# Kernel tuning notes

Hardware: AMD Instinct MI355X
Metric: run time of the kernel (lower is better)

## Reference

```python
import jax, jax.numpy as jnp
import numpy as np

DIM = 512
NUM_HEADS = 8
HEAD_DIM = DIM // NUM_HEADS
SCALE = HEAD_DIM ** -0.5


def setup_inputs() -> dict:
    key = jax.random.key(0)
    k_x, k_qkv, k_proj, k_pb = jax.random.split(key, 4)
    x = jax.random.normal(k_x, (2, 4096, DIM), dtype=jnp.float32)
    # nn.Linear weights: stored as [out, in]; qkv_bias=False so no qkv bias.
    w_qkv = jax.random.normal(k_qkv, (3 * DIM, DIM), dtype=jnp.float32) * (DIM ** -0.5)
    w_proj = jax.random.normal(k_proj, (DIM, DIM), dtype=jnp.float32) * (DIM ** -0.5)
    b_proj = jax.random.normal(k_pb, (DIM,), dtype=jnp.float32) * 0.01
    return {"x": x, "w_qkv": w_qkv, "w_proj": w_proj, "b_proj": b_proj}


def reference(x, w_qkv, w_proj, b_proj):
    B, N, D = x.shape
    H, Hd = NUM_HEADS, HEAD_DIM
    # qkv: [B, N, 3D] -> [3, B, H, N, Hd]
    qkv = (x @ w_qkv.T).reshape(B, N, 3, H, Hd).transpose(2, 0, 3, 1, 4)
    q, k, v = qkv[0], qkv[1], qkv[2]
    # Naive full attention matrix in fp32 (matches original non-fused path).
    attn = jnp.einsum('bhqd,bhkd->bhqk', q, k) * SCALE
    attn = jax.nn.softmax(attn, axis=-1)
    out = jnp.einsum('bhqk,bhkd->bhqd', attn, v)
    out = out.transpose(0, 2, 1, 3).reshape(B, N, D)
    return out @ w_proj.T + b_proj
```

## Files before the change

kernel.cpp:

```cpp
#include <hip/hip_runtime.h>
#include <stdint.h>

#define SEQ   4096
#define DIMM  512
#define HDIM  64
#define NH    8
#define ROWS  8192
#define QKVN  1536

typedef __attribute__((ext_vector_type(8))) __bf16 bf16x8;
typedef __attribute__((ext_vector_type(4))) float  f32x4;
typedef __attribute__((ext_vector_type(2))) uint32_t u32x2;

__device__ __forceinline__ uint16_t f2bfu(float f) {
  uint32_t u = __builtin_bit_cast(uint32_t, f);
  return (uint16_t)((u + 0x7FFFu + ((u >> 16) & 1u)) >> 16);
}

__device__ __forceinline__ f32x4 mfma16(bf16x8 a, bf16x8 b, f32x4 c) {
  return __builtin_amdgcn_mfma_f32_16x16x32_bf16(a, b, c, 0, 0, 0);
}

__device__ __forceinline__ void gld16(const void* g, void* l) {
  __builtin_amdgcn_global_load_lds(
      (const __attribute__((address_space(1))) uint32_t*)g,
      (__attribute__((address_space(3))) uint32_t*)l, 16, 0, 0);
}

#define X4  (ROWS * DIMM / 4)
#define Q4  (QKVN * DIMM / 4)
#define P4  (DIMM * DIMM / 4)

__global__ __launch_bounds__(256) void cvt_kernel(
    const float* __restrict__ x, const float* __restrict__ wq,
    const float* __restrict__ wp, uint16_t* __restrict__ xb,
    uint16_t* __restrict__ wqb, uint16_t* __restrict__ wpb) {
  int idx = blockIdx.x * 256 + threadIdx.x;
  const float* src; uint16_t* dst; int i4;
  if (idx < X4)            { src = x;  dst = xb;  i4 = idx; }
  else if (idx < X4 + Q4)  { src = wq; dst = wqb; i4 = idx - X4; }
  else                     { src = wp; dst = wpb; i4 = idx - X4 - Q4; }
  float4 v = ((const float4*)src)[i4];
  ushort4 o;
  o.x = f2bfu(v.x); o.y = f2bfu(v.y); o.z = f2bfu(v.z); o.w = f2bfu(v.w);
  ((ushort4*)dst)[i4] = o;
}

__device__ __forceinline__ void gemm_core(
    const uint16_t* __restrict__ A, const uint16_t* __restrict__ B,
    uint16_t* As, uint16_t* Bs, f32x4 acc[4][4]) {
  const int tid = threadIdx.x;
  const int lane = tid & 63, wave = tid >> 6;
  const int quad = lane >> 4, l16 = lane & 15;
  const int wr = (wave & 1) * 64, wc = (wave >> 1) * 64;
  const int bm = blockIdx.x, bn = blockIdx.y;
  const int sw = (l16 >> 1) & 3;

  for (int kt = 0; kt < DIMM / 32; ++kt) {
#pragma unroll
    for (int it = 0; it < 2; ++it) {
      int L = it * 256 + tid;
      int r = L >> 2, c = L & 3;
      int gc = c ^ ((r >> 1) & 3);
      int ldsoff = (it * 256 + (tid & ~63)) * 16;
      gld16((const char*)A + ((size_t)(bm * 128 + r) * DIMM + kt * 32) * 2 + gc * 16,
            (char*)As + ldsoff);
      gld16((const char*)B + ((size_t)(bn * 128 + r) * DIMM + kt * 32) * 2 + gc * 16,
            (char*)Bs + ldsoff);
    }
    __syncthreads();
    bf16x8 af[4], bfr[4];
#pragma unroll
    for (int i = 0; i < 4; ++i)
      af[i] = *(const bf16x8*)(As + (wr + i * 16 + l16) * 32 + ((quad ^ sw) * 8));
#pragma unroll
    for (int j = 0; j < 4; ++j)
      bfr[j] = *(const bf16x8*)(Bs + (wc + j * 16 + l16) * 32 + ((quad ^ sw) * 8));
#pragma unroll
    for (int i = 0; i < 4; ++i)
#pragma unroll
      for (int j = 0; j < 4; ++j)
        acc[i][j] = mfma16(af[i], bfr[j], acc[i][j]);
    __syncthreads();
  }
}

__global__ __launch_bounds__(256, 2) void qkv_gemm(
    const uint16_t* __restrict__ xb, const uint16_t* __restrict__ wqb,
    uint16_t* __restrict__ qd, uint16_t* __restrict__ kd,
    uint16_t* __restrict__ vt) {
  __shared__ __align__(16) uint16_t As[128 * 32];
  __shared__ __align__(16) uint16_t Bs[128 * 32];
  f32x4 acc[4][4];
#pragma unroll
  for (int i = 0; i < 4; ++i)
#pragma unroll
    for (int j = 0; j < 4; ++j) acc[i][j] = f32x4{0.f, 0.f, 0.f, 0.f};

  gemm_core(xb, wqb, As, Bs, acc);

  const int lane = threadIdx.x & 63, wave = threadIdx.x >> 6;
  const int quad = lane >> 4, l16 = lane & 15;
  const int wr = (wave & 1) * 64, wc = (wave >> 1) * 64;
#pragma unroll
  for (int i = 0; i < 4; ++i) {
    int m0 = blockIdx.x * 128 + wr + i * 16 + quad * 4;
    int b = m0 >> 12, n0 = m0 & 4095;
#pragma unroll
    for (int j = 0; j < 4; ++j) {
      int jc = blockIdx.y * 128 + wc + j * 16 + l16;
      int region = jc >> 9;
      int h = (jc >> 6) & 7, hd = jc & 63;
      int bh = (b << 3) | h;
      if (region == 0) {
#pragma unroll
        for (int r = 0; r < 4; ++r)
          qd[((size_t)bh * SEQ + n0 + r) * HDIM + hd] = f2bfu(acc[i][j][r] * 0.125f);
      } else if (region == 1) {
#pragma unroll
        for (int r = 0; r < 4; ++r)
          kd[((size_t)bh * SEQ + n0 + r) * HDIM + hd] = f2bfu(acc[i][j][r]);
      } else {
        ushort4 pk;
        pk.x = f2bfu(acc[i][j][0]); pk.y = f2bfu(acc[i][j][1]);
        pk.z = f2bfu(acc[i][j][2]); pk.w = f2bfu(acc[i][j][3]);
        *(ushort4*)(vt + ((size_t)bh * HDIM + hd) * SEQ + n0) = pk;
      }
    }
  }
}

__global__ __launch_bounds__(256, 3) void attn_kernel(
    const uint16_t* __restrict__ qd, const uint16_t* __restrict__ kd,
    const uint16_t* __restrict__ vt, uint16_t* __restrict__ ao) {
  __shared__ __align__(16) uint16_t Ks[128 * 64];
  __shared__ __align__(16) uint16_t Vs[64 * 128];
  __shared__ __align__(16) uint16_t Ps[4][32 * 64];

  const int tid = threadIdx.x, lane = tid & 63, wave = tid >> 6;
  const int quad = lane >> 4, l16 = lane & 15;
  const int qt = blockIdx.x, bh = blockIdx.y;
  const size_t base_qk = (size_t)bh * SEQ * HDIM;
  const size_t base_v  = (size_t)bh * HDIM * SEQ;
  const int sw7 = l16 & 7;
  uint16_t* Pw = &Ps[wave][0];

  bf16x8 qf[2][2];
#pragma unroll
  for (int it2 = 0; it2 < 2; ++it2)
#pragma unroll
    for (int kh = 0; kh < 2; ++kh)
      qf[it2][kh] = *(const bf16x8*)(qd + base_qk +
          (size_t)(qt * 128 + wave * 32 + it2 * 16 + l16) * HDIM + kh * 32 + quad * 8);

  f32x4 O[2][4];
  float lsum[2] = {0.f, 0.f};
#pragma unroll
  for (int a = 0; a < 2; ++a)
#pragma unroll
    for (int d = 0; d < 4; ++d) O[a][d] = f32x4{0.f, 0.f, 0.f, 0.f};

  for (int kt = 0; kt < SEQ / 128; ++kt) {
#pragma unroll
    for (int it = 0; it < 4; ++it) {
      int L = it * 256 + tid;
      int ldsoff = (it * 256 + (tid & ~63)) * 16;
      int rk = L >> 3, ck = L & 7;
      int gck = ck ^ (rk & 7);
      gld16((const char*)kd + (base_qk + (size_t)(kt * 128 + rk) * HDIM) * 2 + gck * 16,
            (char*)Ks + ldsoff);
      int rv = L >> 4, cv = L & 15;
      int gcv = cv ^ (rv & 15);
      gld16((const char*)vt + (base_v + (size_t)rv * SEQ + (size_t)kt * 128) * 2 + gcv * 16,
            (char*)Vs + ldsoff);
    }
    __syncthreads();

#pragma unroll
    for (int half = 0; half < 2; ++half) {
      f32x4 P[4][2];
#pragma unroll
      for (int jh = 0; jh < 4; ++jh) {
        int jf = half * 4 + jh;
        const uint16_t* krow = Ks + (jf * 16 + l16) * 64;
        bf16x8 kf0 = *(const bf16x8*)(krow + ((quad ^ sw7) * 8));
        bf16x8 kf1 = *(const bf16x8*)(krow + (((4 + quad) ^ sw7) * 8));
#pragma unroll
        for (int it2 = 0; it2 < 2; ++it2) {
          f32x4 s = f32x4{0.f, 0.f, 0.f, 0.f};
          s = mfma16(kf0, qf[it2][0], s);
          s = mfma16(kf1, qf[it2][1], s);
          P[jh][it2] = s;
        }
      }

#pragma unroll
      for (int jh = 0; jh < 4; ++jh)
#pragma unroll
        for (int it2 = 0; it2 < 2; ++it2) {
          float p0 = __expf(P[jh][it2][0]);
          float p1 = __expf(P[jh][it2][1]);
          float p2 = __expf(P[jh][it2][2]);
          float p3 = __expf(P[jh][it2][3]);
          lsum[it2] += (p0 + p1) + (p2 + p3);
          uint32_t a0 = __builtin_bit_cast(uint32_t, p0) + 0x8000u;
          uint32_t a1 = __builtin_bit_cast(uint32_t, p1) + 0x8000u;
          uint32_t a2 = __builtin_bit_cast(uint32_t, p2) + 0x8000u;
          uint32_t a3 = __builtin_bit_cast(uint32_t, p3) + 0x8000u;
          u32x2 pk;
          pk.x = (a0 >> 16) | (a1 & 0xFFFF0000u);
          pk.y = (a2 >> 16) | (a3 & 0xFFFF0000u);
          int c16 = (jh * 2 + (quad >> 1)) ^ sw7;
          *(u32x2*)((char*)Pw + (it2 * 16 + l16) * 128 + c16 * 16 + (quad & 1) * 8) = pk;
        }

#pragma unroll
      for (int kp = 0; kp < 2; ++kp) {
        bf16x8 pb[2];
#pragma unroll
        for (int it2 = 0; it2 < 2; ++it2)
          pb[it2] = *(const bf16x8*)((const char*)Pw + (it2 * 16 + l16) * 128 +
                                     (((kp * 4 + quad) ^ sw7) * 16));
        bf16x8 va[4];
#pragma unroll
        for (int dl = 0; dl < 4; ++dl)
          va[dl] = *(const bf16x8*)((const char*)Vs + (dl * 16 + l16) * 256 +
                                    (((half * 8 + kp * 4 + quad) ^ l16) & 15) * 16);
#pragma unroll
        for (int it2 = 0; it2 < 2; ++it2)
#pragma unroll
          for (int dl = 0; dl < 4; ++dl)
            O[it2][dl] = mfma16(va[dl], pb[it2], O[it2][dl]);
      }
    }
    __syncthreads();
  }

  float inv[2];
#pragma unroll
  for (int it2 = 0; it2 < 2; ++it2) {
    float l = lsum[it2];
    l += __shfl_xor(l, 16);
    l += __shfl_xor(l, 32);
    inv[it2] = 1.0f / l;
  }

  const int b = bh >> 3, h = bh & 7;
#pragma unroll
  for (int it2 = 0; it2 < 2; ++it2) {
    int q = qt * 128 + wave * 32 + it2 * 16 + l16;
    size_t rowbase = ((size_t)(b * SEQ + q)) * DIMM + h * HDIM;
#pragma unroll
    for (int dl = 0; dl < 4; ++dl) {
      ushort4 pk;
      pk.x = f2bfu(O[it2][dl][0] * inv[it2]);
      pk.y = f2bfu(O[it2][dl][1] * inv[it2]);
      pk.z = f2bfu(O[it2][dl][2] * inv[it2]);
      pk.w = f2bfu(O[it2][dl][3] * inv[it2]);
      *(ushort4*)(ao + rowbase + dl * 16 + quad * 4) = pk;
    }
  }
}

__global__ __launch_bounds__(256, 2) void proj_gemm(
    const uint16_t* __restrict__ ao, const uint16_t* __restrict__ wpb,
    const float* __restrict__ bprj, float* __restrict__ out) {
  __shared__ __align__(16) uint16_t As[128 * 32];
  __shared__ __align__(16) uint16_t Bs[128 * 32];
  f32x4 acc[4][4];
#pragma unroll
  for (int i = 0; i < 4; ++i)
#pragma unroll
    for (int j = 0; j < 4; ++j) acc[i][j] = f32x4{0.f, 0.f, 0.f, 0.f};

  gemm_core(ao, wpb, As, Bs, acc);

  const int lane = threadIdx.x & 63, wave = threadIdx.x >> 6;
  const int quad = lane >> 4, l16 = lane & 15;
  const int wr = (wave & 1) * 64, wc = (wave >> 1) * 64;
#pragma unroll
  for (int i = 0; i < 4; ++i) {
    int m0 = blockIdx.x * 128 + wr + i * 16 + quad * 4;
#pragma unroll
    for (int j = 0; j < 4; ++j) {
      int jc = blockIdx.y * 128 + wc + j * 16 + l16;
      float bias = bprj[jc];
#pragma unroll
      for (int r = 0; r < 4; ++r)
        out[(size_t)(m0 + r) * DIMM + jc] = acc[i][j][r] + bias;
    }
  }
}

extern "C" void kernel_launch(void* const* d_in, const int* in_sizes, int n_in,
                              void* d_out, int out_size, void* d_ws, size_t ws_size,
                              hipStream_t stream) {
  const float* x     = (const float*)d_in[0];
  const float* wqkv  = (const float*)d_in[1];
  const float* wproj = (const float*)d_in[2];
  const float* bproj = (const float*)d_in[3];

  char* ws = (char*)d_ws;
  uint16_t* xb  = (uint16_t*)(ws + 0);
  uint16_t* wqb = (uint16_t*)(ws + 8388608);
  uint16_t* wpb = (uint16_t*)(ws + 9961472);
  uint16_t* qd  = (uint16_t*)(ws + 10485760);
  uint16_t* kd  = (uint16_t*)(ws + 18874368);
  uint16_t* vt  = (uint16_t*)(ws + 27262976);
  uint16_t* ao  = (uint16_t*)(ws + 35651584);

  cvt_kernel<<<(X4 + Q4 + P4) / 256, 256, 0, stream>>>(x, wqkv, wproj, xb, wqb, wpb);
  qkv_gemm<<<dim3(64, 12), 256, 0, stream>>>(xb, wqb, qd, kd, vt);
  attn_kernel<<<dim3(32, 16), 256, 0, stream>>>(qd, kd, vt, ao);
  proj_gemm<<<dim3(64, 4), 256, 0, stream>>>(ao, wpb, bproj, (float*)d_out);
}
```

Baseline: 208.3 us.

## Split attention key tiles across wave pairs and use exp2 with folded log2e

The attention block grows from 4 to 8 waves. Each pair of waves shares 32 query rows, and each wave in the pair handles one half of every 128-key tile. The partial outputs and row sums are combined through LDS at the end. The Q scale now folds in log2(e) so the softmax can use the native exp2 instruction instead of __expf. This gives more waves per CU to hide latency and cuts the per-wave serial work, at the cost of a larger P buffer in LDS, an extra reduction step with its barrier, and a tighter register budget under the launch bounds of (512, 4).

```diff
diff --git a/kernel.cpp b/kernel.cpp
--- a/kernel.cpp
+++ b/kernel.cpp
@@ -20,6 +20,12 @@
 __device__ __forceinline__ f32x4 mfma16(bf16x8 a, bf16x8 b, f32x4 c) {
   return __builtin_amdgcn_mfma_f32_16x16x32_bf16(a, b, c, 0, 0, 0);
 }
+
+#if __has_builtin(__builtin_amdgcn_exp2f)
+#define EXP2F(x) __builtin_amdgcn_exp2f(x)
+#else
+#define EXP2F(x) exp2f(x)
+#endif
 
 __device__ __forceinline__ void gld16(const void* g, void* l) {
   __builtin_amdgcn_global_load_lds(
@@ -102,6 +108,7 @@
   const int lane = threadIdx.x & 63, wave = threadIdx.x >> 6;
   const int quad = lane >> 4, l16 = lane & 15;
   const int wr = (wave & 1) * 64, wc = (wave >> 1) * 64;
+  const float qscale = 0.125f * 1.44269504f;
 #pragma unroll
   for (int i = 0; i < 4; ++i) {
     int m0 = blockIdx.x * 128 + wr + i * 16 + quad * 4;
@@ -115,7 +122,7 @@
       if (region == 0) {
 #pragma unroll
         for (int r = 0; r < 4; ++r)
-          qd[((size_t)bh * SEQ + n0 + r) * HDIM + hd] = f2bfu(acc[i][j][r] * 0.125f);
+          qd[((size_t)bh * SEQ + n0 + r) * HDIM + hd] = f2bfu(acc[i][j][r] * qscale);
       } else if (region == 1) {
 #pragma unroll
         for (int r = 0; r < 4; ++r)
@@ -130,20 +137,21 @@
   }
 }
 
-__global__ __launch_bounds__(256, 3) void attn_kernel(
+__global__ __launch_bounds__(512, 4) void attn_kernel(
     const uint16_t* __restrict__ qd, const uint16_t* __restrict__ kd,
     const uint16_t* __restrict__ vt, uint16_t* __restrict__ ao) {
   __shared__ __align__(16) uint16_t Ks[128 * 64];
   __shared__ __align__(16) uint16_t Vs[64 * 128];
-  __shared__ __align__(16) uint16_t Ps[4][32 * 64];
+  __shared__ __align__(16) uint16_t Ps[8][32 * 64];
 
   const int tid = threadIdx.x, lane = tid & 63, wave = tid >> 6;
   const int quad = lane >> 4, l16 = lane & 15;
+  const int pair = wave >> 1, khalf = wave & 1;
   const int qt = blockIdx.x, bh = blockIdx.y;
   const size_t base_qk = (size_t)bh * SEQ * HDIM;
   const size_t base_v  = (size_t)bh * HDIM * SEQ;
   const int sw7 = l16 & 7;
-  uint16_t* Pw = &Ps[wave][0];
+  char* Pw = (char*)Ps + wave * 4096;
 
   bf16x8 qf[2][2];
 #pragma unroll
@@ -151,7 +159,7 @@
 #pragma unroll
     for (int kh = 0; kh < 2; ++kh)
       qf[it2][kh] = *(const bf16x8*)(qd + base_qk +
-          (size_t)(qt * 128 + wave * 32 + it2 * 16 + l16) * HDIM + kh * 32 + quad * 8);
+          (size_t)(qt * 128 + pair * 32 + it2 * 16 + l16) * HDIM + kh * 32 + quad * 8);
 
   f32x4 O[2][4];
   float lsum[2] = {0.f, 0.f};
@@ -162,9 +170,9 @@
 
   for (int kt = 0; kt < SEQ / 128; ++kt) {
 #pragma unroll
-    for (int it = 0; it < 4; ++it) {
-      int L = it * 256 + tid;
-      int ldsoff = (it * 256 + (tid & ~63)) * 16;
+    for (int it = 0; it < 2; ++it) {
+      int L = it * 512 + tid;
+      int ldsoff = (it * 512 + (tid & ~63)) * 16;
       int rk = L >> 3, ck = L & 7;
       int gck = ck ^ (rk & 7);
       gld16((const char*)kd + (base_qk + (size_t)(kt * 128 + rk) * HDIM) * 2 + gck * 16,
@@ -176,88 +184,102 @@
     }
     __syncthreads();
 
-#pragma unroll
-    for (int half = 0; half < 2; ++half) {
-      f32x4 P[4][2];
-#pragma unroll
-      for (int jh = 0; jh < 4; ++jh) {
-        int jf = half * 4 + jh;
-        const uint16_t* krow = Ks + (jf * 16 + l16) * 64;
-        bf16x8 kf0 = *(const bf16x8*)(krow + ((quad ^ sw7) * 8));
-        bf16x8 kf1 = *(const bf16x8*)(krow + (((4 + quad) ^ sw7) * 8));
-#pragma unroll
-        for (int it2 = 0; it2 < 2; ++it2) {
-          f32x4 s = f32x4{0.f, 0.f, 0.f, 0.f};
-          s = mfma16(kf0, qf[it2][0], s);
-          s = mfma16(kf1, qf[it2][1], s);
-          P[jh][it2] = s;
-        }
+    f32x4 P[4][2];
+#pragma unroll
+    for (int jh = 0; jh < 4; ++jh) {
+      int jf = khalf * 4 + jh;
+      const uint16_t* krow = Ks + (jf * 16 + l16) * 64;
+      bf16x8 kf0 = *(const bf16x8*)(krow + ((quad ^ sw7) * 8));
+      bf16x8 kf1 = *(const bf16x8*)(krow + (((4 + quad) ^ sw7) * 8));
+#pragma unroll
+      for (int it2 = 0; it2 < 2; ++it2) {
+        f32x4 s = f32x4{0.f, 0.f, 0.f, 0.f};
+        s = mfma16(kf0, qf[it2][0], s);
+        s = mfma16(kf1, qf[it2][1], s);
+        P[jh][it2] = s;
       }
-
-#pragma unroll
-      for (int jh = 0; jh < 4; ++jh)
-#pragma unroll
-        for (int it2 = 0; it2 < 2; ++it2) {
-          float p0 = __expf(P[jh][it2][0]);
-          float p1 = __expf(P[jh][it2][1]);
-          float p2 = __expf(P[jh][it2][2]);
-          float p3 = __expf(P[jh][it2][3]);
-          lsum[it2] += (p0 + p1) + (p2 + p3);
-          uint32_t a0 = __builtin_bit_cast(uint32_t, p0) + 0x8000u;
-          uint32_t a1 = __builtin_bit_cast(uint32_t, p1) + 0x8000u;
-          uint32_t a2 = __builtin_bit_cast(uint32_t, p2) + 0x8000u;
-          uint32_t a3 = __builtin_bit_cast(uint32_t, p3) + 0x8000u;
-          u32x2 pk;
-          pk.x = (a0 >> 16) | (a1 & 0xFFFF0000u);
-          pk.y = (a2 >> 16) | (a3 & 0xFFFF0000u);
-          int c16 = (jh * 2 + (quad >> 1)) ^ sw7;
-          *(u32x2*)((char*)Pw + (it2 * 16 + l16) * 128 + c16 * 16 + (quad & 1) * 8) = pk;
-        }
-
-#pragma unroll
-      for (int kp = 0; kp < 2; ++kp) {
-        bf16x8 pb[2];
-#pragma unroll
-        for (int it2 = 0; it2 < 2; ++it2)
-          pb[it2] = *(const bf16x8*)((const char*)Pw + (it2 * 16 + l16) * 128 +
-                                     (((kp * 4 + quad) ^ sw7) * 16));
-        bf16x8 va[4];
+    }
+
+#pragma unroll
+    for (int jh = 0; jh < 4; ++jh)
+#pragma unroll
+      for (int it2 = 0; it2 < 2; ++it2) {
+        float p0 = EXP2F(P[jh][it2][0]);
+        float p1 = EXP2F(P[jh][it2][1]);
+        float p2 = EXP2F(P[jh][it2][2]);
+        float p3 = EXP2F(P[jh][it2][3]);
+        lsum[it2] += (p0 + p1) + (p2 + p3);
+        uint32_t a0 = __builtin_bit_cast(uint32_t, p0) + 0x8000u;
+        uint32_t a1 = __builtin_bit_cast(uint32_t, p1) + 0x8000u;
+        uint32_t a2 = __builtin_bit_cast(uint32_t, p2) + 0x8000u;
+        uint32_t a3 = __builtin_bit_cast(uint32_t, p3) + 0x8000u;
+        u32x2 pk;
+        pk.x = (a0 >> 16) | (a1 & 0xFFFF0000u);
+        pk.y = (a2 >> 16) | (a3 & 0xFFFF0000u);
+        int c16 = (jh * 2 + (quad >> 1)) ^ sw7;
+        *(u32x2*)(Pw + (it2 * 16 + l16) * 128 + c16 * 16 + (quad & 1) * 8) = pk;
+      }
+
+#pragma unroll
+    for (int kp = 0; kp < 2; ++kp) {
+      bf16x8 pb[2];
+#pragma unroll
+      for (int it2 = 0; it2 < 2; ++it2)
+        pb[it2] = *(const bf16x8*)(Pw + (it2 * 16 + l16) * 128 +
+                                   (((kp * 4 + quad) ^ sw7) * 16));
+      bf16x8 va[4];
+#pragma unroll
+      for (int dl = 0; dl < 4; ++dl)
+        va[dl] = *(const bf16x8*)((const char*)Vs + (dl * 16 + l16) * 256 +
+                                  (((khalf * 8 + kp * 4 + quad) ^ l16) & 15) * 16);
+#pragma unroll
+      for (int it2 = 0; it2 < 2; ++it2)
 #pragma unroll
         for (int dl = 0; dl < 4; ++dl)
-          va[dl] = *(const bf16x8*)((const char*)Vs + (dl * 16 + l16) * 256 +
-                                    (((half * 8 + kp * 4 + quad) ^ l16) & 15) * 16);
-#pragma unroll
-        for (int it2 = 0; it2 < 2; ++it2)
-#pragma unroll
-          for (int dl = 0; dl < 4; ++dl)
-            O[it2][dl] = mfma16(va[dl], pb[it2], O[it2][dl]);
+          O[it2][dl] = mfma16(va[dl], pb[it2], O[it2][dl]);
+    }
+    __syncthreads();
+  }
+
+  if (!(wave & 1)) {
+    f32x4* ob = (f32x4*)((char*)Ps + wave * 4096);
+#pragma unroll
+    for (int it2 = 0; it2 < 2; ++it2)
+#pragma unroll
+      for (int dl = 0; dl < 4; ++dl)
+        ob[(it2 * 4 + dl) * 64 + lane] = O[it2][dl];
+    float2* lb = (float2*)((char*)Ks + pair * 512);
+    lb[lane] = make_float2(lsum[0], lsum[1]);
+  }
+  __syncthreads();
+  if (wave & 1) {
+    const f32x4* ob = (const f32x4*)((char*)Ps + (wave - 1) * 4096);
+    float2 lp = ((const float2*)((char*)Ks + pair * 512))[lane];
+    lsum[0] += lp.x; lsum[1] += lp.y;
+#pragma unroll
+    for (int it2 = 0; it2 < 2; ++it2)
+#pragma unroll
+      for (int dl = 0; dl < 4; ++dl)
+        O[it2][dl] += ob[(it2 * 4 + dl) * 64 + lane];
+
+    const int b = bh >> 3, h = bh & 7;
+#pragma unroll
+    for (int it2 = 0; it2 < 2; ++it2) {
+      float l = lsum[it2];
+      l += __shfl_xor(l, 16);
+      l += __shfl_xor(l, 32);
+      float inv = 1.0f / l;
+      int q = qt * 128 + pair * 32 + it2 * 16 + l16;
+      size_t rowbase = ((size_t)(b * SEQ + q)) * DIMM + h * HDIM;
+#pragma unroll
+      for (int dl = 0; dl < 4; ++dl) {
+        ushort4 pk;
+        pk.x = f2bfu(O[it2][dl][0] * inv);
+        pk.y = f2bfu(O[it2][dl][1] * inv);
+        pk.z = f2bfu(O[it2][dl][2] * inv);
+        pk.w = f2bfu(O[it2][dl][3] * inv);
+        *(ushort4*)(ao + rowbase + dl * 16 + quad * 4) = pk;
       }
-    }
-    __syncthreads();
-  }
-
-  float inv[2];
-#pragma unroll
-  for (int it2 = 0; it2 < 2; ++it2) {
-    float l = lsum[it2];
-    l += __shfl_xor(l, 16);
-    l += __shfl_xor(l, 32);
-    inv[it2] = 1.0f / l;
-  }
-
-  const int b = bh >> 3, h = bh & 7;
-#pragma unroll
-  for (int it2 = 0; it2 < 2; ++it2) {
-    int q = qt * 128 + wave * 32 + it2 * 16 + l16;
-    size_t rowbase = ((size_t)(b * SEQ + q)) * DIMM + h * HDIM;
-#pragma unroll
-    for (int dl = 0; dl < 4; ++dl) {
-      ushort4 pk;
-      pk.x = f2bfu(O[it2][dl][0] * inv[it2]);
-      pk.y = f2bfu(O[it2][dl][1] * inv[it2]);
-      pk.z = f2bfu(O[it2][dl][2] * inv[it2]);
-      pk.w = f2bfu(O[it2][dl][3] * inv[it2]);
-      *(ushort4*)(ao + rowbase + dl * 16 + quad * 4) = pk;
     }
   }
 }
@@ -311,6 +333,6 @@
 
   cvt_kernel<<<(X4 + Q4 + P4) / 256, 256, 0, stream>>>(x, wqkv, wproj, xb, wqb, wpb);
   qkv_gemm<<<dim3(64, 12), 256, 0, stream>>>(xb, wqb, qd, kd, vt);
-  attn_kernel<<<dim3(32, 16), 256, 0, stream>>>(qd, kd, vt, ao);
+  attn_kernel<<<dim3(32, 16), 512, 0, stream>>>(qd, kd, vt, ao);
   proj_gemm<<<dim3(64, 4), 256, 0, stream>>>(ao, wpb, bproj, (float*)d_out);
 }
```

Result: faster. 195.1 us (-6.3%).
